# Kernel optimization log

Hardware: AMD Instinct MI355X
Metric: run time of the kernel (lower is better)

Reference implementation:

```python
import jax, jax.numpy as jnp
import numpy as np

EMBED = 768
HEADS = 12
FFN = 3072
EPS = 1e-5

def _linear_params(key, din, dout):
    k1, k2 = jax.random.split(key)
    s = 1.0 / np.sqrt(din)
    W = jax.random.uniform(k1, (din, dout), minval=-s, maxval=s, dtype=jnp.float32)
    b = jax.random.uniform(k2, (dout,), minval=-s, maxval=s, dtype=jnp.float32)
    return W, b

def setup_inputs() -> dict:
    key = jax.random.key(0)
    ks = jax.random.split(key, 8)
    x = jax.random.normal(ks[0], (1, 4096, EMBED), dtype=jnp.float32)
    Wq, bq = _linear_params(ks[1], EMBED, EMBED)
    Wk, bk = _linear_params(ks[2], EMBED, EMBED)
    Wv, bv = _linear_params(ks[3], EMBED, EMBED)
    Wo, bo = _linear_params(ks[4], EMBED, EMBED)
    W1, b1 = _linear_params(ks[5], EMBED, FFN)
    W2, b2 = _linear_params(ks[6], FFN, EMBED)
    ln1_g = jnp.ones((EMBED,), jnp.float32); ln1_b = jnp.zeros((EMBED,), jnp.float32)
    ln2_g = jnp.ones((EMBED,), jnp.float32); ln2_b = jnp.zeros((EMBED,), jnp.float32)
    return {"x": x, "Wq": Wq, "bq": bq, "Wk": Wk, "bk": bk, "Wv": Wv, "bv": bv,
            "Wo": Wo, "bo": bo, "ln1_g": ln1_g, "ln1_b": ln1_b,
            "ln2_g": ln2_g, "ln2_b": ln2_b, "W1": W1, "b1": b1, "W2": W2, "b2": b2}

def _layernorm(x, g, b):
    mu = jnp.mean(x, axis=-1, keepdims=True)
    var = jnp.mean(jnp.square(x - mu), axis=-1, keepdims=True)
    return (x - mu) * jax.lax.rsqrt(var + EPS) * g + b

def _block(x, Wq, bq, Wk, bk, Wv, bv, Wo, bo, ln1_g, ln1_b, ln2_g, ln2_b, W1, b1, W2, b2):
    B, T, C = x.shape
    H = HEADS
    D = C // H
    # pre-LN
    h = _layernorm(x, ln1_g, ln1_b)
    # naive causal self-attention with explicit [B,H,T,T] scores (as in source)
    q = (h @ Wq + bq).reshape(B, T, H, D).transpose(0, 2, 1, 3)  # bhtd
    k = (h @ Wk + bk).reshape(B, T, H, D).transpose(0, 2, 1, 3)
    v = (h @ Wv + bv).reshape(B, T, H, D).transpose(0, 2, 1, 3)
    scores = jnp.einsum('bhqd,bhkd->bhqk', q, k) / jnp.sqrt(jnp.float32(D))
    causal = jnp.tril(jnp.ones((T, T), dtype=bool))  # True = keep
    scores = jnp.where(causal, scores, -jnp.inf)
    attn = jax.nn.softmax(scores, axis=-1)
    ctx = jnp.einsum('bhqk,bhkd->bhqd', attn, v)
    ctx = ctx.transpose(0, 2, 1, 3).reshape(B, T, C)
    y = ctx @ Wo + bo
    x = y + h  # residual onto ln1 output (source adds to post-LN x)
    # second LN + MLP
    h2 = _layernorm(x, ln2_g, ln2_b)
    m = jax.nn.gelu(h2 @ W1 + b1, approximate=False) @ W2 + b2
    return m + h2

def reference(x, Wq, bq, Wk, bk, Wv, bv, Wo, bo, ln1_g, ln1_b, ln2_g, ln2_b, W1, b1, W2, b2):
    return _block(x, Wq, bq, Wk, bk, Wv, bv, Wo, bo, ln1_g, ln1_b, ln2_g, ln2_b, W1, b1, W2, b2)
```

## Files before the change

kernel.cpp:

```cpp
#include <hip/hip_runtime.h>
#include <math.h>

#define EMBED 768
#define FFN_D 3072
#define TSEQ 4096
#define NHEAD 12
#define DHEAD 64
#define CQKV 2304
#define NSPLIT 4
#define NQITEMS 192
#define SC2Q 0.180336880111120419f

typedef _Float16 f16;
typedef __attribute__((ext_vector_type(2))) _Float16 f16x2;
typedef __attribute__((ext_vector_type(4))) _Float16 f16x4;
typedef __attribute__((ext_vector_type(8))) _Float16 f16x8;
typedef __attribute__((ext_vector_type(4))) float f32x4;

#if __has_builtin(__builtin_amdgcn_exp2f)
#define EXP2(x) __builtin_amdgcn_exp2f(x)
#else
#define EXP2(x) exp2f(x)
#endif

__device__ __forceinline__ f16x2 pkrtz(float a, float b) {
    return __builtin_bit_cast(f16x2, __builtin_amdgcn_cvt_pkrtz(a, b));
}

__device__ __forceinline__ void gload16(const f16* g, f16* lds) {
    __builtin_amdgcn_global_load_lds((const __attribute__((address_space(1))) void*)g,
                                     (__attribute__((address_space(3))) void*)lds, 16, 0, 0);
}

__global__ __launch_bounds__(256) void prep_kernel(const float* __restrict__ Wq,
                                                   const float* __restrict__ Wk,
                                                   const float* __restrict__ Wv,
                                                   const float* __restrict__ Wo,
                                                   const float* __restrict__ W1,
                                                   const float* __restrict__ W2,
                                                   const float* __restrict__ bq,
                                                   const float* __restrict__ bk,
                                                   const float* __restrict__ bv,
                                                   f16* __restrict__ WqkvT,
                                                   f16* __restrict__ WoT,
                                                   f16* __restrict__ W1T,
                                                   f16* __restrict__ W2T,
                                                   float* __restrict__ bqkv) {
    const int b = blockIdx.x;
    const int t = threadIdx.x;
    if (b == 6912) {
#pragma unroll
        for (int i = 0; i < 9; i++) {
            int idx = i * 256 + t;
            if (idx < 768) bqkv[idx] = bq[idx];
            else if (idx < 1536) bqkv[idx] = bk[idx - 768];
            else if (idx < 2304) bqkv[idx] = bv[idx - 1536];
        }
        return;
    }
    const float* W; f16* WT; int din, dout, local;
    if (b < 576)       { W = Wq; WT = WqkvT;                         din = 768;  dout = 768;  local = b; }
    else if (b < 1152) { W = Wk; WT = WqkvT + 768 * 768;             din = 768;  dout = 768;  local = b - 576; }
    else if (b < 1728) { W = Wv; WT = WqkvT + 2 * 768 * 768;         din = 768;  dout = 768;  local = b - 1152; }
    else if (b < 2304) { W = Wo; WT = WoT;                           din = 768;  dout = 768;  local = b - 1728; }
    else if (b < 4608) { W = W1; WT = W1T;                           din = 768;  dout = 3072; local = b - 2304; }
    else               { W = W2; WT = W2T;                           din = 3072; dout = 768;  local = b - 4608; }
    const int tx2 = dout / 32;
    const int j0 = (local % tx2) * 32;
    const int i0 = (local / tx2) * 32;
    __shared__ float tile[32][33];
    const int tx = t & 31;
    const int ty = t >> 5;
#pragma unroll
    for (int rr = ty; rr < 32; rr += 8)
        tile[rr][tx] = W[(size_t)(i0 + rr) * dout + j0 + tx];
    __syncthreads();
#pragma unroll
    for (int rr = ty; rr < 32; rr += 8)
        WT[(size_t)(j0 + rr) * din + i0 + tx] = (f16)tile[tx][rr];
}

__global__ __launch_bounds__(256) void ln_kernel(const float* __restrict__ x,
                                                 const float* __restrict__ g,
                                                 const float* __restrict__ b,
                                                 f16* __restrict__ hh) {
    const int row = blockIdx.x;
    const float* xr = x + (size_t)row * EMBED;
    const int t = threadIdx.x;
    float v0 = xr[t], v1 = xr[t + 256], v2 = xr[t + 512];
    float s = v0 + v1 + v2;
#pragma unroll
    for (int m = 1; m < 64; m <<= 1) s += __shfl_xor(s, m);
    __shared__ float red[4], red2[4];
    const int wid = t >> 6, lane = t & 63;
    if (lane == 0) red[wid] = s;
    __syncthreads();
    float mean = (red[0] + red[1] + red[2] + red[3]) * (1.0f / 768.0f);
    float d0 = v0 - mean, d1 = v1 - mean, d2 = v2 - mean;
    float ss = d0 * d0 + d1 * d1 + d2 * d2;
#pragma unroll
    for (int m = 1; m < 64; m <<= 1) ss += __shfl_xor(ss, m);
    if (lane == 0) red2[wid] = ss;
    __syncthreads();
    float inv = rsqrtf((red2[0] + red2[1] + red2[2] + red2[3]) * (1.0f / 768.0f) + 1e-5f);
    size_t base = (size_t)row * EMBED;
    hh[base + t]       = (f16)(d0 * inv * g[t] + b[t]);
    hh[base + t + 256] = (f16)(d1 * inv * g[t + 256] + b[t + 256]);
    hh[base + t + 512] = (f16)(d2 * inv * g[t + 512] + b[t + 512]);
}

template <int EPI, int BM, int BN>
__global__ __launch_bounds__(256) void gemm_kernel(const f16* __restrict__ A,
                                                   const f16* __restrict__ BT,
                                                   const float* __restrict__ bias,
                                                   const f16* __restrict__ resh,
                                                   float* __restrict__ outf,
                                                   f16* __restrict__ outh,
                                                   f16* __restrict__ vtout,
                                                   int M, int N, int K) {
    constexpr int IM = BM / 32;
    constexpr int JN = BN / 32;
    __shared__ __align__(16) f16 As[BM][64];
    __shared__ __align__(16) f16 Bs[BN][64];
    const int t = threadIdx.x;
    const int m0 = blockIdx.y * BM;
    const int n0 = blockIdx.x * BN;
    const int wid = t >> 6;
    const int lane = t & 63;
    const int wm = (wid >> 1) * (BM / 2);
    const int wn = (wid & 1) * (BN / 2);
    const int lr = lane & 15;
    const int quad = lane >> 4;
    const int sr = lane >> 3;
    const int scn = (lane & 7) ^ sr;
    const int xv = lr & 7;

    f32x4 zero = {0.f, 0.f, 0.f, 0.f};
    f32x4 acc[IM][JN];
#pragma unroll
    for (int i = 0; i < IM; i++)
#pragma unroll
        for (int j = 0; j < JN; j++) acc[i][j] = zero;

    const f16* Ap = A + (size_t)(m0 + wid * (BM / 4) + sr) * K + scn * 8;
    const f16* Bp = BT + (size_t)(n0 + wid * (BN / 4) + sr) * K + scn * 8;

    for (int k0 = 0; k0 < K; k0 += 64) {
        __syncthreads();
#pragma unroll
        for (int c = 0; c < BM / 32; c++)
            gload16(Ap + (size_t)(c * 8) * K + k0, &As[wid * (BM / 4) + c * 8][0]);
#pragma unroll
        for (int c = 0; c < BN / 32; c++)
            gload16(Bp + (size_t)(c * 8) * K + k0, &Bs[wid * (BN / 4) + c * 8][0]);
        __syncthreads();
#pragma unroll
        for (int ks = 0; ks < 2; ks++) {
            f16x8 af[IM], bf[JN];
#pragma unroll
            for (int i = 0; i < IM; i++)
                af[i] = *(const f16x8*)&As[wm + i * 16 + lr][((ks * 4 + quad) ^ xv) * 8];
#pragma unroll
            for (int j = 0; j < JN; j++)
                bf[j] = *(const f16x8*)&Bs[wn + j * 16 + lr][((ks * 4 + quad) ^ xv) * 8];
#pragma unroll
            for (int i = 0; i < IM; i++)
#pragma unroll
                for (int j = 0; j < JN; j++)
                    acc[i][j] = __builtin_amdgcn_mfma_f32_16x16x32_f16(bf[j], af[i], acc[i][j], 0, 0, 0);
        }
    }

    const bool vsec = (EPI == 0) && (n0 >= 2 * EMBED);
#pragma unroll
    for (int i = 0; i < IM; i++) {
        const int row = m0 + wm + i * 16 + lr;
#pragma unroll
        for (int j = 0; j < JN; j++) {
            const int col = n0 + wn + j * 16 + quad * 4;
            const float4 bv = *(const float4*)&bias[col];
            float v0 = acc[i][j][0] + bv.x;
            float v1 = acc[i][j][1] + bv.y;
            float v2 = acc[i][j][2] + bv.z;
            float v3 = acc[i][j][3] + bv.w;
            const size_t idx = (size_t)row * N + col;
            if (EPI == 0) {
                if (vsec) {
                    const int c0 = col - 2 * EMBED;
                    vtout[(size_t)(c0 + 0) * TSEQ + row] = (f16)v0;
                    vtout[(size_t)(c0 + 1) * TSEQ + row] = (f16)v1;
                    vtout[(size_t)(c0 + 2) * TSEQ + row] = (f16)v2;
                    vtout[(size_t)(c0 + 3) * TSEQ + row] = (f16)v3;
                } else {
                    const float qs = (col < EMBED) ? SC2Q : 1.0f;
                    f16x4 hv = {(f16)(v0 * qs), (f16)(v1 * qs), (f16)(v2 * qs), (f16)(v3 * qs)};
                    *(f16x4*)&outh[idx] = hv;
                }
            } else if (EPI == 1) {
                const f16x4 rr = *(const f16x4*)&resh[idx];
                f32x4 ov = {v0 + (float)rr[0], v1 + (float)rr[1], v2 + (float)rr[2], v3 + (float)rr[3]};
                *(f32x4*)&outf[idx] = ov;
            } else {
                f16x4 hv = {(f16)(0.5f * v0 * (1.0f + erff(v0 * 0.70710678118654752f))),
                            (f16)(0.5f * v1 * (1.0f + erff(v1 * 0.70710678118654752f))),
                            (f16)(0.5f * v2 * (1.0f + erff(v2 * 0.70710678118654752f))),
                            (f16)(0.5f * v3 * (1.0f + erff(v3 * 0.70710678118654752f)))};
                *(f16x4*)&outh[idx] = hv;
            }
        }
    }
}

__global__ __launch_bounds__(256) void attn_kernel(const f16* __restrict__ qkv,
                                                   const f16* __restrict__ vT,
                                                   f16* __restrict__ OpartH,
                                                   float2* __restrict__ ml,
                                                   int* __restrict__ ctr) {
    __shared__ __align__(16) f16 Ks[64][72];
    __shared__ __align__(16) f16 Vt[64][72];
    __shared__ int s_item;
    const int t = threadIdx.x;
    const int wid = t >> 6;
    const int lane = t & 63;
    const int lr = lane & 15;
    const int quad = lane >> 4;
    const int srow = t >> 3;
    const int scol = (t & 7) * 8;
    const int pA = (t & 1) * 16 + ((t >> 1) & 1) * 4 + (t & 4) * 8;
    const int xq = blockIdx.x & 7;

    for (;;) {
        __syncthreads();
        if (t == 0) s_item = atomicAdd(&ctr[xq], 1);
        __syncthreads();
        const int item = s_item;
        if (item >= NQITEMS) return;
        const int qb = 31 - item / 6;
        const int u = xq * 6 + item % 6;
        const int h = u >> 2;
        const int sp = u & 3;
        const int q0 = qb * 128;

        const int nkb = 2 * qb + 2;
        const int chunk = (nkb + NSPLIT - 1) / NSPLIT;
        const int kb0 = sp * chunk;
        const int kb1 = min(nkb, kb0 + chunk);
        const int wrow0 = q0 + wid * 32;

        float m_i[2] = {-INFINITY, -INFINITY};
        float l_lane[2] = {0.f, 0.f};
        f32x4 zero = {0.f, 0.f, 0.f, 0.f};
        f32x4 o[4][2];
#pragma unroll
        for (int dt = 0; dt < 4; dt++)
#pragma unroll
            for (int qt = 0; qt < 2; qt++) o[dt][qt] = zero;

        f16x8 qf[2][2];
        int4 kreg[2], vreg[2];
        const f16* kbase = qkv + EMBED + (size_t)h * DHEAD;
        const f16* vbase = vT + (size_t)h * DHEAD * TSEQ;
        if (kb0 < kb1) {
#pragma unroll
            for (int qt = 0; qt < 2; qt++)
#pragma unroll
                for (int dh = 0; dh < 2; dh++)
                    qf[qt][dh] = *(const f16x8*)(qkv + (size_t)(wrow0 + qt * 16 + lr) * CQKV
                                                 + h * DHEAD + dh * 32 + quad * 8);
            const int k0 = kb0 * 64;
#pragma unroll
            for (int p = 0; p < 2; p++) {
                kreg[p] = *(const int4*)(kbase + (size_t)(k0 + p * 32 + srow) * CQKV + scol);
                vreg[p] = *(const int4*)(vbase + (size_t)(p * 32 + srow) * TSEQ + k0 + scol);
            }
        }

        for (int kb = kb0; kb < kb1; ++kb) {
            const int k0 = kb * 64;
            __syncthreads();
#pragma unroll
            for (int p = 0; p < 2; p++) {
                *(int4*)&Ks[p * 32 + srow][scol] = kreg[p];
                *(int2*)&Vt[p * 32 + srow][pA]     = make_int2(vreg[p].x, vreg[p].y);
                *(int2*)&Vt[p * 32 + srow][pA + 8] = make_int2(vreg[p].z, vreg[p].w);
            }
            __syncthreads();
            if (kb + 1 < kb1) {
                const int kn = (kb + 1) * 64;
#pragma unroll
                for (int p = 0; p < 2; p++) {
                    kreg[p] = *(const int4*)(kbase + (size_t)(kn + p * 32 + srow) * CQKV + scol);
                    vreg[p] = *(const int4*)(vbase + (size_t)(p * 32 + srow) * TSEQ + kn + scol);
                }
            }

            if (k0 <= wrow0 + 31) {
                f32x4 s[4][2];
#pragma unroll
                for (int kt = 0; kt < 4; kt++)
#pragma unroll
                    for (int qt = 0; qt < 2; qt++) s[kt][qt] = zero;
#pragma unroll
                for (int dh = 0; dh < 2; dh++) {
#pragma unroll
                    for (int kt = 0; kt < 4; kt++) {
                        f16x8 kf = *(const f16x8*)&Ks[kt * 16 + lr][dh * 32 + quad * 8];
#pragma unroll
                        for (int qt = 0; qt < 2; qt++)
                            s[kt][qt] = __builtin_amdgcn_mfma_f32_16x16x32_f16(kf, qf[qt][dh], s[kt][qt], 0, 0, 0);
                    }
                }
                if (k0 + 63 > wrow0) {
#pragma unroll
                    for (int kt = 0; kt < 4; kt++)
#pragma unroll
                        for (int qt = 0; qt < 2; qt++)
#pragma unroll
                            for (int r = 0; r < 4; r++) {
                                int key = k0 + kt * 16 + quad * 4 + r;
                                int row = wrow0 + qt * 16 + lr;
                                if (key > row) s[kt][qt][r] = -INFINITY;
                            }
                }
                float mx[2];
#pragma unroll
                for (int qt = 0; qt < 2; qt++) {
                    float m = -INFINITY;
#pragma unroll
                    for (int kt = 0; kt < 4; kt++)
#pragma unroll
                        for (int r = 0; r < 4; r++) m = fmaxf(m, s[kt][qt][r]);
                    m = fmaxf(m, __shfl_xor(m, 16));
                    m = fmaxf(m, __shfl_xor(m, 32));
                    mx[qt] = m;
                }
                if (__any((mx[0] > m_i[0] + 4.f) || (mx[1] > m_i[1] + 4.f))) {
#pragma unroll
                    for (int qt = 0; qt < 2; qt++) {
                        float mn = fmaxf(m_i[qt], mx[qt]);
                        float al = EXP2(m_i[qt] - mn);
                        m_i[qt] = mn;
                        l_lane[qt] *= al;
#pragma unroll
                        for (int dt = 0; dt < 4; dt++)
#pragma unroll
                            for (int r = 0; r < 4; r++) o[dt][qt][r] *= al;
                    }
                }
                union PW { f16x8 v8; f16x2 h2[4]; };
                PW pw[2][2];
                float rs[2] = {0.f, 0.f};
#pragma unroll
                for (int kt = 0; kt < 4; kt++)
#pragma unroll
                    for (int qt = 0; qt < 2; qt++) {
                        float p0 = EXP2(s[kt][qt][0] - m_i[qt]);
                        float p1 = EXP2(s[kt][qt][1] - m_i[qt]);
                        float p2 = EXP2(s[kt][qt][2] - m_i[qt]);
                        float p3 = EXP2(s[kt][qt][3] - m_i[qt]);
                        rs[qt] += (p0 + p1) + (p2 + p3);
                        pw[kt >> 1][qt].h2[(kt & 1) * 2]     = pkrtz(p0, p1);
                        pw[kt >> 1][qt].h2[(kt & 1) * 2 + 1] = pkrtz(p2, p3);
                    }
#pragma unroll
                for (int qt = 0; qt < 2; qt++) l_lane[qt] += rs[qt];
#pragma unroll
                for (int s2 = 0; s2 < 2; s2++)
#pragma unroll
                    for (int dt = 0; dt < 4; dt++) {
                        f16x8 vf = *(const f16x8*)&Vt[dt * 16 + lr][s2 * 32 + quad * 8];
#pragma unroll
                        for (int qt = 0; qt < 2; qt++)
                            o[dt][qt] = __builtin_amdgcn_mfma_f32_16x16x32_f16(vf, pw[s2][qt].v8, o[dt][qt], 0, 0, 0);
                    }
            }
        }

        float l_i[2];
#pragma unroll
        for (int qt = 0; qt < 2; qt++) {
            float v2 = l_lane[qt];
            v2 += __shfl_xor(v2, 16);
            v2 += __shfl_xor(v2, 32);
            l_i[qt] = v2;
        }
        __syncthreads();
        f16* ob = ((wid & 2) ? &Vt[0][0] : &Ks[0][0]) + (wid & 1) * (32 * 72);
#pragma unroll
        for (int qt = 0; qt < 2; qt++)
#pragma unroll
            for (int dt = 0; dt < 4; dt++) {
                f16x4 oh = {(f16)o[dt][qt][0], (f16)o[dt][qt][1], (f16)o[dt][qt][2], (f16)o[dt][qt][3]};
                *(f16x4*)&ob[(qt * 16 + lr) * 72 + dt * 16 + quad * 4] = oh;
            }
        const int rl = lane >> 3;
        const int ck = lane & 7;
#pragma unroll
        for (int i = 0; i < 4; i++) {
            const int row_l = rl + i * 8;
            f16x8 val = *(const f16x8*)&ob[row_l * 72 + ck * 8];
            *(f16x8*)&OpartH[((size_t)sp * TSEQ + wrow0 + row_l) * EMBED + h * DHEAD + ck * 8] = val;
        }
#pragma unroll
        for (int qt = 0; qt < 2; qt++)
            if (quad == 0) {
                int row = wrow0 + qt * 16 + lr;
                ml[((size_t)sp * TSEQ + row) * NHEAD + h] = make_float2(m_i[qt], l_i[qt]);
            }
    }
}

__global__ __launch_bounds__(256) void attn_merge_kernel(const f16* __restrict__ OpartH,
                                                         const float2* __restrict__ ml,
                                                         f16* __restrict__ ctx) {
    const int row = blockIdx.x;
    const int t = threadIdx.x;
    __shared__ float wgt[NSPLIT][NHEAD];
    if (t < NHEAD) {
        float m[NSPLIT], l[NSPLIT];
        float M = -INFINITY;
#pragma unroll
        for (int s = 0; s < NSPLIT; s++) {
            float2 v = ml[((size_t)s * TSEQ + row) * NHEAD + t];
            m[s] = v.x; l[s] = v.y;
            M = fmaxf(M, m[s]);
        }
        float L = 0.f;
        float w[NSPLIT];
#pragma unroll
        for (int s = 0; s < NSPLIT; s++) {
            w[s] = exp2f(m[s] - M);
            L += l[s] * w[s];
        }
        float rL = 1.0f / L;
#pragma unroll
        for (int s = 0; s < NSPLIT; s++) wgt[s][t] = w[s] * rL;
    }
    __syncthreads();
#pragma unroll
    for (int p = 0; p < 3; p++) {
        int c = t + p * 256;
        int h = c >> 6;
        float acc = 0.f;
#pragma unroll
        for (int s = 0; s < NSPLIT; s++)
            acc += wgt[s][h] * (float)OpartH[((size_t)s * TSEQ + row) * EMBED + c];
        ctx[(size_t)row * EMBED + c] = (f16)acc;
    }
}

extern "C" void kernel_launch(void* const* d_in, const int* in_sizes, int n_in,
                              void* d_out, int out_size, void* d_ws, size_t ws_size,
                              hipStream_t stream) {
    const float* x     = (const float*)d_in[0];
    const float* Wq    = (const float*)d_in[1];
    const float* bq    = (const float*)d_in[2];
    const float* Wk    = (const float*)d_in[3];
    const float* bk    = (const float*)d_in[4];
    const float* Wv    = (const float*)d_in[5];
    const float* bv    = (const float*)d_in[6];
    const float* Wo    = (const float*)d_in[7];
    const float* bo    = (const float*)d_in[8];
    const float* ln1_g = (const float*)d_in[9];
    const float* ln1_b = (const float*)d_in[10];
    const float* ln2_g = (const float*)d_in[11];
    const float* ln2_b = (const float*)d_in[12];
    const float* W1    = (const float*)d_in[13];
    const float* b1    = (const float*)d_in[14];
    const float* W2    = (const float*)d_in[15];
    const float* b2    = (const float*)d_in[16];

    char* p = (char*)d_ws;
    auto alloc = [&](size_t bytes) -> void* {
        void* r = (void*)p;
        p += (bytes + 255) & ~(size_t)255;
        return r;
    };
    f16*   WqkvT = (f16*)alloc((size_t)CQKV * EMBED * 2);
    f16*   WoT   = (f16*)alloc((size_t)EMBED * EMBED * 2);
    f16*   W1T   = (f16*)alloc((size_t)FFN_D * EMBED * 2);
    f16*   W2T   = (f16*)alloc((size_t)EMBED * FFN_D * 2);
    float* bqkv  = (float*)alloc((size_t)CQKV * 4);
    f16*   hh    = (f16*)alloc((size_t)TSEQ * EMBED * 2);
    f16*   qkv   = (f16*)alloc((size_t)TSEQ * CQKV * 2);
    f16*   vT    = (f16*)alloc((size_t)EMBED * TSEQ * 2);
    f16*   ctx   = (f16*)alloc((size_t)TSEQ * EMBED * 2);
    float* x2    = (float*)alloc((size_t)TSEQ * EMBED * 4);
    f16*   h2h   = (f16*)alloc((size_t)TSEQ * EMBED * 2);
    f16*   m1    = (f16*)alloc((size_t)TSEQ * FFN_D * 2);
    int*   ctr   = (int*)alloc(256);

    f16*    OpartH = m1;
    float2* mlbuf  = (float2*)x2;

    dim3 blk(256);
    prep_kernel<<<dim3(6913), blk, 0, stream>>>(Wq, Wk, Wv, Wo, W1, W2, bq, bk, bv,
                                                WqkvT, WoT, W1T, W2T, bqkv);
    ln_kernel<<<dim3(TSEQ), blk, 0, stream>>>(x, ln1_g, ln1_b, hh);
    gemm_kernel<0, 128, 128><<<dim3(CQKV / 128, TSEQ / 128), blk, 0, stream>>>(
        hh, WqkvT, bqkv, nullptr, nullptr, qkv, vT, TSEQ, CQKV, EMBED);
    (void)hipMemsetAsync(ctr, 0, 256, stream);
    attn_kernel<<<dim3(768), blk, 0, stream>>>(qkv, vT, OpartH, mlbuf, ctr);
    attn_merge_kernel<<<dim3(TSEQ), blk, 0, stream>>>(OpartH, mlbuf, ctx);
    gemm_kernel<1, 128, 64><<<dim3(EMBED / 64, TSEQ / 128), blk, 0, stream>>>(
        ctx, WoT, bo, hh, x2, nullptr, nullptr, TSEQ, EMBED, EMBED);
    ln_kernel<<<dim3(TSEQ), blk, 0, stream>>>(x2, ln2_g, ln2_b, h2h);
    gemm_kernel<2, 128, 128><<<dim3(FFN_D / 128, TSEQ / 128), blk, 0, stream>>>(
        h2h, W1T, b1, nullptr, nullptr, m1, nullptr, TSEQ, FFN_D, EMBED);
    gemm_kernel<1, 128, 64><<<dim3(EMBED / 64, TSEQ / 128), blk, 0, stream>>>(
        m1, W2T, b2, h2h, (float*)d_out, nullptr, nullptr, TSEQ, EMBED, FFN_D);
}
```

Baseline: 329.6 us.

## Double-buffer attention K/V tiles, widen transpose tiles, vectorize merge, retile GEMMs

The attention kernel now double-buffers K/V in shared memory, so one barrier per key block suffices, and raises MFMA wave priority with s_setprio. The weight-transpose prep kernel moves to 64x64 tiles with packed f16x2 stores, and the merge kernel uses 128 threads with 8-wide vector loads. The attention grid grows to 1024 persistent blocks, and the two N=768 GEMMs switch from 128x64 to 128x128 tiles. This trades more LDS per block and fewer GEMM blocks, which lowers occupancy and wave count, for less synchronization and better data reuse.

```diff
diff --git a/kernel.cpp b/kernel.cpp
--- a/kernel.cpp
+++ b/kernel.cpp
@@ -48,7 +48,7 @@
                                                    float* __restrict__ bqkv) {
     const int b = blockIdx.x;
     const int t = threadIdx.x;
-    if (b == 6912) {
+    if (b == 1728) {
 #pragma unroll
         for (int i = 0; i < 9; i++) {
             int idx = i * 256 + t;
@@ -59,25 +59,29 @@
         return;
     }
     const float* W; f16* WT; int din, dout, local;
-    if (b < 576)       { W = Wq; WT = WqkvT;                         din = 768;  dout = 768;  local = b; }
-    else if (b < 1152) { W = Wk; WT = WqkvT + 768 * 768;             din = 768;  dout = 768;  local = b - 576; }
-    else if (b < 1728) { W = Wv; WT = WqkvT + 2 * 768 * 768;         din = 768;  dout = 768;  local = b - 1152; }
-    else if (b < 2304) { W = Wo; WT = WoT;                           din = 768;  dout = 768;  local = b - 1728; }
-    else if (b < 4608) { W = W1; WT = W1T;                           din = 768;  dout = 3072; local = b - 2304; }
-    else               { W = W2; WT = W2T;                           din = 3072; dout = 768;  local = b - 4608; }
-    const int tx2 = dout / 32;
-    const int j0 = (local % tx2) * 32;
-    const int i0 = (local / tx2) * 32;
-    __shared__ float tile[32][33];
-    const int tx = t & 31;
-    const int ty = t >> 5;
-#pragma unroll
-    for (int rr = ty; rr < 32; rr += 8)
+    if (b < 144)       { W = Wq; WT = WqkvT;                 din = 768;  dout = 768;  local = b; }
+    else if (b < 288)  { W = Wk; WT = WqkvT + 768 * 768;     din = 768;  dout = 768;  local = b - 144; }
+    else if (b < 432)  { W = Wv; WT = WqkvT + 2 * 768 * 768; din = 768;  dout = 768;  local = b - 288; }
+    else if (b < 576)  { W = Wo; WT = WoT;                   din = 768;  dout = 768;  local = b - 432; }
+    else if (b < 1152) { W = W1; WT = W1T;                   din = 768;  dout = 3072; local = b - 576; }
+    else               { W = W2; WT = W2T;                   din = 3072; dout = 768;  local = b - 1152; }
+    const int ntx = dout / 64;
+    const int j0 = (local % ntx) * 64;
+    const int i0 = (local / ntx) * 64;
+    __shared__ float tile[64][65];
+    const int tx = t & 63;
+    const int ty = t >> 6;
+#pragma unroll
+    for (int rr = ty; rr < 64; rr += 4)
         tile[rr][tx] = W[(size_t)(i0 + rr) * dout + j0 + tx];
     __syncthreads();
-#pragma unroll
-    for (int rr = ty; rr < 32; rr += 8)
-        WT[(size_t)(j0 + rr) * din + i0 + tx] = (f16)tile[tx][rr];
+    const int half = t & 31;
+    const int rw = t >> 5;
+#pragma unroll
+    for (int rr = rw; rr < 64; rr += 8) {
+        f16x2 v = {(f16)tile[2 * half][rr], (f16)tile[2 * half + 1][rr]};
+        *(f16x2*)&WT[(size_t)(j0 + rr) * din + i0 + 2 * half] = v;
+    }
 }
 
 __global__ __launch_bounds__(256) void ln_kernel(const float* __restrict__ x,
@@ -216,8 +220,8 @@
                                                    f16* __restrict__ OpartH,
                                                    float2* __restrict__ ml,
                                                    int* __restrict__ ctr) {
-    __shared__ __align__(16) f16 Ks[64][72];
-    __shared__ __align__(16) f16 Vt[64][72];
+    __shared__ __align__(16) f16 Ks[2][64][72];
+    __shared__ __align__(16) f16 Vt[2][64][72];
     __shared__ int s_item;
     const int t = threadIdx.x;
     const int wid = t >> 6;
@@ -273,26 +277,42 @@
                 kreg[p] = *(const int4*)(kbase + (size_t)(k0 + p * 32 + srow) * CQKV + scol);
                 vreg[p] = *(const int4*)(vbase + (size_t)(p * 32 + srow) * TSEQ + k0 + scol);
             }
-        }
-
-        for (int kb = kb0; kb < kb1; ++kb) {
-            const int k0 = kb * 64;
-            __syncthreads();
 #pragma unroll
             for (int p = 0; p < 2; p++) {
-                *(int4*)&Ks[p * 32 + srow][scol] = kreg[p];
-                *(int2*)&Vt[p * 32 + srow][pA]     = make_int2(vreg[p].x, vreg[p].y);
-                *(int2*)&Vt[p * 32 + srow][pA + 8] = make_int2(vreg[p].z, vreg[p].w);
-            }
-            __syncthreads();
-            if (kb + 1 < kb1) {
-                const int kn = (kb + 1) * 64;
+                *(int4*)&Ks[0][p * 32 + srow][scol] = kreg[p];
+                *(int2*)&Vt[0][p * 32 + srow][pA]     = make_int2(vreg[p].x, vreg[p].y);
+                *(int2*)&Vt[0][p * 32 + srow][pA + 8] = make_int2(vreg[p].z, vreg[p].w);
+            }
+            if (kb0 + 1 < kb1) {
+                const int kn = k0 + 64;
 #pragma unroll
                 for (int p = 0; p < 2; p++) {
                     kreg[p] = *(const int4*)(kbase + (size_t)(kn + p * 32 + srow) * CQKV + scol);
                     vreg[p] = *(const int4*)(vbase + (size_t)(p * 32 + srow) * TSEQ + kn + scol);
                 }
             }
+        }
+        __syncthreads();
+
+        int bsel = 0;
+        for (int kb = kb0; kb < kb1; ++kb, bsel ^= 1) {
+            const int k0 = kb * 64;
+            if (kb + 1 < kb1) {
+#pragma unroll
+                for (int p = 0; p < 2; p++) {
+                    *(int4*)&Ks[bsel ^ 1][p * 32 + srow][scol] = kreg[p];
+                    *(int2*)&Vt[bsel ^ 1][p * 32 + srow][pA]     = make_int2(vreg[p].x, vreg[p].y);
+                    *(int2*)&Vt[bsel ^ 1][p * 32 + srow][pA + 8] = make_int2(vreg[p].z, vreg[p].w);
+                }
+                if (kb + 2 < kb1) {
+                    const int kn = (kb + 2) * 64;
+#pragma unroll
+                    for (int p = 0; p < 2; p++) {
+                        kreg[p] = *(const int4*)(kbase + (size_t)(kn + p * 32 + srow) * CQKV + scol);
+                        vreg[p] = *(const int4*)(vbase + (size_t)(p * 32 + srow) * TSEQ + kn + scol);
+                    }
+                }
+            }
 
             if (k0 <= wrow0 + 31) {
                 f32x4 s[4][2];
@@ -300,16 +320,18 @@
                 for (int kt = 0; kt < 4; kt++)
 #pragma unroll
                     for (int qt = 0; qt < 2; qt++) s[kt][qt] = zero;
+                __builtin_amdgcn_s_setprio(1);
 #pragma unroll
                 for (int dh = 0; dh < 2; dh++) {
 #pragma unroll
                     for (int kt = 0; kt < 4; kt++) {
-                        f16x8 kf = *(const f16x8*)&Ks[kt * 16 + lr][dh * 32 + quad * 8];
+                        f16x8 kf = *(const f16x8*)&Ks[bsel][kt * 16 + lr][dh * 32 + quad * 8];
 #pragma unroll
                         for (int qt = 0; qt < 2; qt++)
                             s[kt][qt] = __builtin_amdgcn_mfma_f32_16x16x32_f16(kf, qf[qt][dh], s[kt][qt], 0, 0, 0);
                     }
                 }
+                __builtin_amdgcn_s_setprio(0);
                 if (k0 + 63 > wrow0) {
 #pragma unroll
                     for (int kt = 0; kt < 4; kt++)
@@ -364,16 +386,19 @@
                     }
 #pragma unroll
                 for (int qt = 0; qt < 2; qt++) l_lane[qt] += rs[qt];
+                __builtin_amdgcn_s_setprio(1);
 #pragma unroll
                 for (int s2 = 0; s2 < 2; s2++)
 #pragma unroll
                     for (int dt = 0; dt < 4; dt++) {
-                        f16x8 vf = *(const f16x8*)&Vt[dt * 16 + lr][s2 * 32 + quad * 8];
+                        f16x8 vf = *(const f16x8*)&Vt[bsel][dt * 16 + lr][s2 * 32 + quad * 8];
 #pragma unroll
                         for (int qt = 0; qt < 2; qt++)
                             o[dt][qt] = __builtin_amdgcn_mfma_f32_16x16x32_f16(vf, pw[s2][qt].v8, o[dt][qt], 0, 0, 0);
                     }
-            }
+                __builtin_amdgcn_s_setprio(0);
+            }
+            __syncthreads();
         }
 
         float l_i[2];
@@ -384,8 +409,7 @@
             v2 += __shfl_xor(v2, 32);
             l_i[qt] = v2;
         }
-        __syncthreads();
-        f16* ob = ((wid & 2) ? &Vt[0][0] : &Ks[0][0]) + (wid & 1) * (32 * 72);
+        f16* ob = &Ks[0][0][0] + wid * (32 * 72);
 #pragma unroll
         for (int qt = 0; qt < 2; qt++)
 #pragma unroll
@@ -410,7 +434,7 @@
     }
 }
 
-__global__ __launch_bounds__(256) void attn_merge_kernel(const f16* __restrict__ OpartH,
+__global__ __launch_bounds__(128) void attn_merge_kernel(const f16* __restrict__ OpartH,
                                                          const float2* __restrict__ ml,
                                                          f16* __restrict__ ctx) {
     const int row = blockIdx.x;
@@ -437,15 +461,20 @@
         for (int s = 0; s < NSPLIT; s++) wgt[s][t] = w[s] * rL;
     }
     __syncthreads();
-#pragma unroll
-    for (int p = 0; p < 3; p++) {
-        int c = t + p * 256;
-        int h = c >> 6;
-        float acc = 0.f;
-#pragma unroll
-        for (int s = 0; s < NSPLIT; s++)
-            acc += wgt[s][h] * (float)OpartH[((size_t)s * TSEQ + row) * EMBED + c];
-        ctx[(size_t)row * EMBED + c] = (f16)acc;
+    if (t < 96) {
+        const int h = t >> 3;
+        float acc[8] = {0.f, 0.f, 0.f, 0.f, 0.f, 0.f, 0.f, 0.f};
+#pragma unroll
+        for (int s = 0; s < NSPLIT; s++) {
+            const float w = wgt[s][h];
+            f16x8 v = *(const f16x8*)&OpartH[((size_t)s * TSEQ + row) * EMBED + t * 8];
+#pragma unroll
+            for (int e = 0; e < 8; e++) acc[e] += w * (float)v[e];
+        }
+        f16x8 out;
+#pragma unroll
+        for (int e = 0; e < 8; e++) out[e] = (f16)acc[e];
+        *(f16x8*)&ctx[(size_t)row * EMBED + t * 8] = out;
     }
 }
 
@@ -494,19 +523,19 @@
     float2* mlbuf  = (float2*)x2;
 
     dim3 blk(256);
-    prep_kernel<<<dim3(6913), blk, 0, stream>>>(Wq, Wk, Wv, Wo, W1, W2, bq, bk, bv,
+    prep_kernel<<<dim3(1729), blk, 0, stream>>>(Wq, Wk, Wv, Wo, W1, W2, bq, bk, bv,
                                                 WqkvT, WoT, W1T, W2T, bqkv);
     ln_kernel<<<dim3(TSEQ), blk, 0, stream>>>(x, ln1_g, ln1_b, hh);
     gemm_kernel<0, 128, 128><<<dim3(CQKV / 128, TSEQ / 128), blk, 0, stream>>>(
         hh, WqkvT, bqkv, nullptr, nullptr, qkv, vT, TSEQ, CQKV, EMBED);
     (void)hipMemsetAsync(ctr, 0, 256, stream);
-    attn_kernel<<<dim3(768), blk, 0, stream>>>(qkv, vT, OpartH, mlbuf, ctr);
-    attn_merge_kernel<<<dim3(TSEQ), blk, 0, stream>>>(OpartH, mlbuf, ctx);
-    gemm_kernel<1, 128, 64><<<dim3(EMBED / 64, TSEQ / 128), blk, 0, stream>>>(
+    attn_kernel<<<dim3(1024), blk, 0, stream>>>(qkv, vT, OpartH, mlbuf, ctr);
+    attn_merge_kernel<<<dim3(TSEQ), dim3(128), 0, stream>>>(OpartH, mlbuf, ctx);
+    gemm_kernel<1, 128, 128><<<dim3(EMBED / 128, TSEQ / 128), blk, 0, stream>>>(
         ctx, WoT, bo, hh, x2, nullptr, nullptr, TSEQ, EMBED, EMBED);
     ln_kernel<<<dim3(TSEQ), blk, 0, stream>>>(x2, ln2_g, ln2_b, h2h);
     gemm_kernel<2, 128, 128><<<dim3(FFN_D / 128, TSEQ / 128), blk, 0, stream>>>(
         h2h, W1T, b1, nullptr, nullptr, m1, nullptr, TSEQ, FFN_D, EMBED);
-    gemm_kernel<1, 128, 64><<<dim3(EMBED / 64, TSEQ / 128), blk, 0, stream>>>(
+    gemm_kernel<1, 128, 128><<<dim3(EMBED / 128, TSEQ / 128), blk, 0, stream>>>(
         m1, W2T, b2, h2h, (float*)d_out, nullptr, nullptr, TSEQ, EMBED, FFN_D);
 }
```

Measured after the change: 353.2 us. 1.07x slower.
